# Kernel optimization log

Measured on AMD Instinct MI355X. Metric: run time of the kernel, lower is better.

## Reference

```python
import jax, jax.numpy as jnp
import numpy as np

B, N, F_IN, F_OUT = 64, 1024, 128, 64
NEG_BIG = -9e15


def setup_inputs() -> dict:
    key = jax.random.key(0)
    k1, k2, k3, k4 = jax.random.split(key, 4)
    atoms_vector = jax.random.normal(k1, (B, N, F_IN), dtype=jnp.float32)
    adjacency = jax.random.randint(k2, (B, N, N), 0, 2, dtype=jnp.int32)
    # xavier_uniform-ish init for params
    W = jax.random.uniform(k3, (F_IN, F_OUT), dtype=jnp.float32, minval=-1.0, maxval=1.0) * (1.414 * np.sqrt(6.0 / (F_IN + F_OUT)))
    a = jax.random.uniform(k4, (2 * F_OUT, 1), dtype=jnp.float32, minval=-1.0, maxval=1.0) * (1.414 * np.sqrt(6.0 / (2 * F_OUT + 1)))
    return {"atoms_vector": atoms_vector, "adjacency": adjacency, "W": W, "a": a}


def reference(atoms_vector, adjacency, W, a):
    f_out = W.shape[1]
    Wh = jnp.einsum('bni,io->bno', atoms_vector, W)  # (B, N, F_OUT)
    # The repeat_interleave/cat construction computes e[b,i,j] =
    # leaky_relu(a1 . Wh[b,i] + a2 . Wh[b,j]) — separable, so compute it directly.
    a1 = a[:f_out, 0]   # (F_OUT,)
    a2 = a[f_out:, 0]   # (F_OUT,)
    s1 = Wh @ a1        # (B, N)
    s2 = Wh @ a2        # (B, N)
    e = jax.nn.leaky_relu(s1[:, :, None] + s2[:, None, :], negative_slope=0.1)  # (B,N,N)
    attention = jnp.where(adjacency > 0, e, jnp.float32(NEG_BIG))
    attention = jax.nn.softmax(attention, axis=2)
    h_prime = jnp.einsum('bij,bjf->bif', attention, Wh)  # (B, N, F_OUT)
    return jax.nn.elu(h_prime)
```

## Files before the change

### kernel.cpp

```cpp
#include <hip/hip_runtime.h>
#include <hip/hip_bf16.h>

#define NN   1024
#define FIN  128
#define FOUT 64

typedef __attribute__((ext_vector_type(8))) short short8;
typedef __attribute__((ext_vector_type(4))) float f32x4;

__device__ inline unsigned short f2bf(float x) {
    union { __hip_bfloat16 h; unsigned short u; } c;
    c.h = __float2bfloat16(x);
    return c.u;
}
__device__ inline unsigned packbf(float a, float b) {
    return (unsigned)f2bf(a) | ((unsigned)f2bf(b) << 16);
}

__global__ __launch_bounds__(256) void k1_proj(
    const float* __restrict__ X, const float* __restrict__ W,
    const float* __restrict__ a,
    unsigned short* __restrict__ whbt,
    float* __restrict__ s1g, float* __restrict__ s2g)
{
    __shared__ float Ws[FIN][FOUT];
    __shared__ float Xs[64][FIN + 4];
    __shared__ unsigned short Ob[FOUT][64];

    const int t = threadIdx.x;
    const int blk = blockIdx.x;
    const int b = blk >> 4;
    const int r0 = (blk & 15) << 6;
    const float* Xg = X + ((size_t)(b * NN + r0)) * FIN;

    const float4* Wg4 = (const float4*)W;
    #pragma unroll
    for (int i = 0; i < 8; ++i) {
        int idx = t + i * 256;
        float4 v = Wg4[idx];
        int kk = idx >> 4, oo = (idx & 15) << 2;
        *(float4*)&Ws[kk][oo] = v;
    }
    #pragma unroll
    for (int i = 0; i < 8; ++i) {
        int idx = t + i * 256;
        float4 v = ((const float4*)Xg)[idx];
        int rr = idx >> 5, cc = (idx & 31) << 2;
        *(float4*)&Xs[rr][cc] = v;
    }
    __syncthreads();

    const int l = t & 63, w = t >> 6;
    const int c0 = (l & 15) << 2;
    const int rs = l >> 4;
    const int rbase = w * 16 + rs * 4;

    float acc[4][4] = {};
    for (int k = 0; k < FIN; ++k) {
        float4 wv = *(const float4*)&Ws[k][c0];
        #pragma unroll
        for (int q = 0; q < 4; ++q) {
            float x = Xs[rbase + q][k];
            acc[q][0] += x * wv.x; acc[q][1] += x * wv.y;
            acc[q][2] += x * wv.z; acc[q][3] += x * wv.w;
        }
    }

    float a1v[4], a2v[4];
    #pragma unroll
    for (int c = 0; c < 4; ++c) { a1v[c] = a[c0 + c]; a2v[c] = a[FOUT + c0 + c]; }
    #pragma unroll
    for (int q = 0; q < 4; ++q) {
        float p1 = acc[q][0]*a1v[0] + acc[q][1]*a1v[1] + acc[q][2]*a1v[2] + acc[q][3]*a1v[3];
        float p2 = acc[q][0]*a2v[0] + acc[q][1]*a2v[1] + acc[q][2]*a2v[2] + acc[q][3]*a2v[3];
        #pragma unroll
        for (int m = 1; m <= 8; m <<= 1) {
            p1 += __shfl_xor(p1, m, 64);
            p2 += __shfl_xor(p2, m, 64);
        }
        if ((l & 15) == 0) {
            int row = r0 + rbase + q;
            s1g[b * NN + row] = p1;
            s2g[b * NN + row] = p2;
        }
    }

    #pragma unroll
    for (int q = 0; q < 4; ++q)
        #pragma unroll
        for (int c = 0; c < 4; ++c)
            Ob[c0 + c][rbase + q] = f2bf(acc[q][c]);
    __syncthreads();

    {
        int o = t >> 2, rseg = (t & 3) << 4;
        unsigned short* dst = whbt + ((size_t)(b * FOUT + o)) * NN + r0 + rseg;
        const unsigned short* sp = &Ob[o][rseg];
        *(float4*)dst       = *(const float4*)sp;
        *(float4*)(dst + 8) = *(const float4*)(sp + 8);
    }
}

__global__ __launch_bounds__(256) void k1b_max(
    const float* __restrict__ s2g, float* __restrict__ s2max)
{
    int b = blockIdx.x, t = threadIdx.x;
    float m = -3.4e38f;
    #pragma unroll
    for (int i = 0; i < 4; ++i) m = fmaxf(m, s2g[b * NN + t + i * 256]);
    #pragma unroll
    for (int d = 1; d <= 32; d <<= 1) m = fmaxf(m, __shfl_xor(m, d, 64));
    __shared__ float red[4];
    if ((t & 63) == 0) red[t >> 6] = m;
    __syncthreads();
    if (t == 0) s2max[b] = fmaxf(fmaxf(red[0], red[1]), fmaxf(red[2], red[3]));
}

__global__ __launch_bounds__(256) void k2_attn(
    const int* __restrict__ adj,
    const unsigned short* __restrict__ whbt,
    const float* __restrict__ s1g, const float* __restrict__ s2g,
    const float* __restrict__ s2maxg,
    float* __restrict__ outg)
{
    const int t = threadIdx.x, l = t & 63, w = t >> 6;
    const int bid = blockIdx.x;
    const int b = bid >> 4;
    const int i0 = (bid & 15) << 6;
    const int r16 = l & 15;
    const int jo = (l >> 4) << 3;
    const int row = i0 + w * 16 + r16;

    const float s2m = s2maxg[b];
    const float s1v = s1g[b * NN + row];
    const float tt = s1v + s2m;
    const float Mr = fmaxf(tt, 0.1f * tt);

    const int* adjr = adj + (size_t)b * NN * NN + (size_t)row * NN;
    const float* s2r = s2g + b * NN;
    const unsigned short* wb = whbt + (size_t)b * FOUT * NN + (size_t)r16 * NN;

    f32x4 acc[4];
    #pragma unroll
    for (int s = 0; s < 4; ++s)
        #pragma unroll
        for (int r = 0; r < 4; ++r) acc[s][r] = 0.f;
    float den = 0.f;

    #pragma unroll 2
    for (int jt = 0; jt < NN; jt += 32) {
        const int j0 = jt + jo;
        int4 a0 = *(const int4*)(adjr + j0);
        int4 a1 = *(const int4*)(adjr + j0 + 4);
        float4 sa = *(const float4*)(s2r + j0);
        float4 sb = *(const float4*)(s2r + j0 + 4);
        short8 bf[4];
        #pragma unroll
        for (int s = 0; s < 4; ++s)
            bf[s] = *(const short8*)(wb + (size_t)s * (16 * NN) + j0);

        const float sv[8] = {sa.x, sa.y, sa.z, sa.w, sb.x, sb.y, sb.z, sb.w};
        const int   am[8] = {a0.x, a0.y, a0.z, a0.w, a1.x, a1.y, a1.z, a1.w};
        unsigned pk[4];
        #pragma unroll
        for (int e = 0; e < 4; ++e) {
            float xa = s1v + sv[2*e];
            float xb = s1v + sv[2*e+1];
            float ea = fmaxf(xa, 0.1f * xa) - Mr;
            float eb = fmaxf(xb, 0.1f * xb) - Mr;
            float pa = am[2*e]   > 0 ? __expf(ea) : 0.f;
            float pb = am[2*e+1] > 0 ? __expf(eb) : 0.f;
            den += pa + pb;
            pk[e] = packbf(pa, pb);
        }
        union { unsigned u[4]; short8 s8; } A;
        A.u[0] = pk[0]; A.u[1] = pk[1]; A.u[2] = pk[2]; A.u[3] = pk[3];
        #pragma unroll
        for (int s = 0; s < 4; ++s)
            acc[s] = __builtin_amdgcn_mfma_f32_16x16x32_bf16(A.s8, bf[s], acc[s], 0, 0, 0);
    }

    den += __shfl_xor(den, 16, 64);
    den += __shfl_xor(den, 32, 64);

    const int rb = (l >> 4) << 2;
    float inv[4];
    #pragma unroll
    for (int rr = 0; rr < 4; ++rr) {
        float dd = __shfl(den, rb + rr, 64);
        inv[rr] = dd > 0.f ? 1.f / dd : 0.f;
    }
    float* orow = outg + ((size_t)(b * NN + i0 + w * 16 + rb)) * FOUT;
    #pragma unroll
    for (int s = 0; s < 4; ++s)
        #pragma unroll
        for (int rr = 0; rr < 4; ++rr) {
            float v = acc[s][rr] * inv[rr];
            float res = v > 0.f ? v : (__expf(v) - 1.f);
            orow[(size_t)rr * FOUT + s * 16 + r16] = res;
        }
}

extern "C" void kernel_launch(void* const* d_in, const int* in_sizes, int n_in,
                              void* d_out, int out_size, void* d_ws, size_t ws_size,
                              hipStream_t stream) {
    const float* atoms = (const float*)d_in[0];
    const int*   adj   = (const int*)d_in[1];
    const float* W     = (const float*)d_in[2];
    const float* a     = (const float*)d_in[3];
    float* out = (float*)d_out;

    unsigned short* whbt = (unsigned short*)d_ws;
    float* s1g    = (float*)((char*)d_ws + (8u << 20));
    float* s2g    = (float*)((char*)d_ws + (8u << 20) + (256u << 10));
    float* s2maxg = (float*)((char*)d_ws + (8u << 20) + (512u << 10));

    k1_proj<<<1024, 256, 0, stream>>>(atoms, W, a, whbt, s1g, s2g);
    k1b_max<<<64, 256, 0, stream>>>(s2g, s2maxg);
    k2_attn<<<1024, 256, 0, stream>>>(adj, whbt, s1g, s2g, s2maxg, out);
}
```

Before: 127.8 us.

## Use MFMA bf16 for projection, fold attention vector into W, batch adjacency loads

Adds a tiny prep kernel that computes W·a1 and W·a2 and a transposed bf16 copy of W. The projection kernel then computes s1/s2 directly from X in fp32 and Wh with bf16 MFMA instructions, replacing the LDS-staged scalar FMA GEMM and the shared-memory transpose. The attention kernel now issues the adjacency loads for four 32-column chunks up front per 128-column step, to expose more memory-level parallelism. This trades fp32 accuracy for bf16 in Wh inputs and adds an extra kernel launch.

```diff
diff --git a/kernel.cpp b/kernel.cpp
--- a/kernel.cpp
+++ b/kernel.cpp
@@ -16,88 +16,93 @@
 __device__ inline unsigned packbf(float a, float b) {
     return (unsigned)f2bf(a) | ((unsigned)f2bf(b) << 16);
 }
+__device__ inline float dot4(float4 x, float4 y) {
+    return x.x*y.x + x.y*y.y + x.z*y.z + x.w*y.w;
+}
+
+__global__ __launch_bounds__(256) void k0_prep(
+    const float* __restrict__ W, const float* __restrict__ a,
+    float* __restrict__ wa1, float* __restrict__ wa2,
+    unsigned short* __restrict__ wtbf)
+{
+    const int t = threadIdx.x;
+    if (t < FIN) {
+        float s1 = 0.f, s2 = 0.f;
+        #pragma unroll
+        for (int c = 0; c < FOUT; c += 4) {
+            float4 wv  = *(const float4*)(W + t * FOUT + c);
+            float4 a1v = *(const float4*)(a + c);
+            float4 a2v = *(const float4*)(a + FOUT + c);
+            s1 += dot4(wv, a1v);
+            s2 += dot4(wv, a2v);
+        }
+        wa1[t] = s1; wa2[t] = s2;
+    }
+    const int col = t >> 2, ks = (t & 3) << 5;
+    #pragma unroll
+    for (int k = 0; k < 32; ++k)
+        wtbf[col * FIN + ks + k] = f2bf(W[(size_t)(ks + k) * FOUT + col]);
+}
 
 __global__ __launch_bounds__(256) void k1_proj(
-    const float* __restrict__ X, const float* __restrict__ W,
-    const float* __restrict__ a,
+    const float* __restrict__ X,
+    const float* __restrict__ wa1, const float* __restrict__ wa2,
+    const unsigned short* __restrict__ wtbf,
     unsigned short* __restrict__ whbt,
     float* __restrict__ s1g, float* __restrict__ s2g)
 {
-    __shared__ float Ws[FIN][FOUT];
-    __shared__ float Xs[64][FIN + 4];
-    __shared__ unsigned short Ob[FOUT][64];
-
-    const int t = threadIdx.x;
-    const int blk = blockIdx.x;
-    const int b = blk >> 4;
-    const int r0 = (blk & 15) << 6;
-    const float* Xg = X + ((size_t)(b * NN + r0)) * FIN;
-
-    const float4* Wg4 = (const float4*)W;
-    #pragma unroll
-    for (int i = 0; i < 8; ++i) {
-        int idx = t + i * 256;
-        float4 v = Wg4[idx];
-        int kk = idx >> 4, oo = (idx & 15) << 2;
-        *(float4*)&Ws[kk][oo] = v;
-    }
-    #pragma unroll
-    for (int i = 0; i < 8; ++i) {
-        int idx = t + i * 256;
-        float4 v = ((const float4*)Xg)[idx];
-        int rr = idx >> 5, cc = (idx & 31) << 2;
-        *(float4*)&Xs[rr][cc] = v;
-    }
-    __syncthreads();
-
-    const int l = t & 63, w = t >> 6;
-    const int c0 = (l & 15) << 2;
-    const int rs = l >> 4;
-    const int rbase = w * 16 + rs * 4;
-
-    float acc[4][4] = {};
-    for (int k = 0; k < FIN; ++k) {
-        float4 wv = *(const float4*)&Ws[k][c0];
-        #pragma unroll
-        for (int q = 0; q < 4; ++q) {
-            float x = Xs[rbase + q][k];
-            acc[q][0] += x * wv.x; acc[q][1] += x * wv.y;
-            acc[q][2] += x * wv.z; acc[q][3] += x * wv.w;
-        }
-    }
-
-    float a1v[4], a2v[4];
-    #pragma unroll
-    for (int c = 0; c < 4; ++c) { a1v[c] = a[c0 + c]; a2v[c] = a[FOUT + c0 + c]; }
-    #pragma unroll
-    for (int q = 0; q < 4; ++q) {
-        float p1 = acc[q][0]*a1v[0] + acc[q][1]*a1v[1] + acc[q][2]*a1v[2] + acc[q][3]*a1v[3];
-        float p2 = acc[q][0]*a2v[0] + acc[q][1]*a2v[1] + acc[q][2]*a2v[2] + acc[q][3]*a2v[3];
-        #pragma unroll
-        for (int m = 1; m <= 8; m <<= 1) {
-            p1 += __shfl_xor(p1, m, 64);
-            p2 += __shfl_xor(p2, m, 64);
-        }
-        if ((l & 15) == 0) {
-            int row = r0 + rbase + q;
-            s1g[b * NN + row] = p1;
-            s2g[b * NN + row] = p2;
-        }
-    }
-
-    #pragma unroll
-    for (int q = 0; q < 4; ++q)
-        #pragma unroll
-        for (int c = 0; c < 4; ++c)
-            Ob[c0 + c][rbase + q] = f2bf(acc[q][c]);
-    __syncthreads();
-
-    {
-        int o = t >> 2, rseg = (t & 3) << 4;
-        unsigned short* dst = whbt + ((size_t)(b * FOUT + o)) * NN + r0 + rseg;
-        const unsigned short* sp = &Ob[o][rseg];
-        *(float4*)dst       = *(const float4*)sp;
-        *(float4*)(dst + 8) = *(const float4*)(sp + 8);
+    const int t = threadIdx.x, l = t & 63, w = t >> 6;
+    const int bid = blockIdx.x;
+    const int b = bid >> 4;
+    const int r0 = (bid & 15) << 6;
+    const int r16 = l & 15;
+    const int jo = (l >> 4) << 3;
+    const int row = r0 + w * 16 + r16;
+    const float* xr = X + (size_t)(b * NN + row) * FIN;
+
+    f32x4 acc[4];
+    #pragma unroll
+    for (int s = 0; s < 4; ++s)
+        #pragma unroll
+        for (int r = 0; r < 4; ++r) acc[s][r] = 0.f;
+    float s1p = 0.f, s2p = 0.f;
+
+    #pragma unroll
+    for (int kc = 0; kc < 4; ++kc) {
+        const int k0i = kc * 32 + jo;
+        float4 xa = *(const float4*)(xr + k0i);
+        float4 xb = *(const float4*)(xr + k0i + 4);
+        float4 w1a = *(const float4*)(wa1 + k0i);
+        float4 w1b = *(const float4*)(wa1 + k0i + 4);
+        float4 w2a = *(const float4*)(wa2 + k0i);
+        float4 w2b = *(const float4*)(wa2 + k0i + 4);
+        s1p += dot4(xa, w1a) + dot4(xb, w1b);
+        s2p += dot4(xa, w2a) + dot4(xb, w2b);
+
+        union { unsigned u[4]; short8 s8; } A;
+        A.u[0] = packbf(xa.x, xa.y); A.u[1] = packbf(xa.z, xa.w);
+        A.u[2] = packbf(xb.x, xb.y); A.u[3] = packbf(xb.z, xb.w);
+        #pragma unroll
+        for (int s = 0; s < 4; ++s) {
+            short8 bfv = *(const short8*)(wtbf + (s * 16 + r16) * FIN + k0i);
+            acc[s] = __builtin_amdgcn_mfma_f32_16x16x32_bf16(A.s8, bfv, acc[s], 0, 0, 0);
+        }
+    }
+
+    s1p += __shfl_xor(s1p, 16, 64); s1p += __shfl_xor(s1p, 32, 64);
+    s2p += __shfl_xor(s2p, 16, 64); s2p += __shfl_xor(s2p, 32, 64);
+    if (jo == 0) {
+        s1g[b * NN + row] = s1p;
+        s2g[b * NN + row] = s2p;
+    }
+
+    const int rb = (l >> 4) << 2;
+    #pragma unroll
+    for (int s = 0; s < 4; ++s) {
+        unsigned d0 = packbf(acc[s][0], acc[s][1]);
+        unsigned d1 = packbf(acc[s][2], acc[s][3]);
+        *(uint2*)(whbt + (size_t)(b * FOUT + s * 16 + r16) * NN + r0 + w * 16 + rb)
+            = make_uint2(d0, d1);
     }
 }
 
@@ -147,37 +152,44 @@
         for (int r = 0; r < 4; ++r) acc[s][r] = 0.f;
     float den = 0.f;
 
-    #pragma unroll 2
-    for (int jt = 0; jt < NN; jt += 32) {
-        const int j0 = jt + jo;
-        int4 a0 = *(const int4*)(adjr + j0);
-        int4 a1 = *(const int4*)(adjr + j0 + 4);
-        float4 sa = *(const float4*)(s2r + j0);
-        float4 sb = *(const float4*)(s2r + j0 + 4);
-        short8 bf[4];
-        #pragma unroll
-        for (int s = 0; s < 4; ++s)
-            bf[s] = *(const short8*)(wb + (size_t)s * (16 * NN) + j0);
-
-        const float sv[8] = {sa.x, sa.y, sa.z, sa.w, sb.x, sb.y, sb.z, sb.w};
-        const int   am[8] = {a0.x, a0.y, a0.z, a0.w, a1.x, a1.y, a1.z, a1.w};
-        unsigned pk[4];
-        #pragma unroll
-        for (int e = 0; e < 4; ++e) {
-            float xa = s1v + sv[2*e];
-            float xb = s1v + sv[2*e+1];
-            float ea = fmaxf(xa, 0.1f * xa) - Mr;
-            float eb = fmaxf(xb, 0.1f * xb) - Mr;
-            float pa = am[2*e]   > 0 ? __expf(ea) : 0.f;
-            float pb = am[2*e+1] > 0 ? __expf(eb) : 0.f;
-            den += pa + pb;
-            pk[e] = packbf(pa, pb);
-        }
-        union { unsigned u[4]; short8 s8; } A;
-        A.u[0] = pk[0]; A.u[1] = pk[1]; A.u[2] = pk[2]; A.u[3] = pk[3];
-        #pragma unroll
-        for (int s = 0; s < 4; ++s)
-            acc[s] = __builtin_amdgcn_mfma_f32_16x16x32_bf16(A.s8, bf[s], acc[s], 0, 0, 0);
+    for (int jt = 0; jt < NN; jt += 128) {
+        int4 A0[4], A1[4];
+        #pragma unroll
+        for (int c = 0; c < 4; ++c) {
+            A0[c] = *(const int4*)(adjr + jt + c * 32 + jo);
+            A1[c] = *(const int4*)(adjr + jt + c * 32 + jo + 4);
+        }
+        #pragma unroll
+        for (int c = 0; c < 4; ++c) {
+            const int j0 = jt + c * 32 + jo;
+            float4 sa = *(const float4*)(s2r + j0);
+            float4 sb = *(const float4*)(s2r + j0 + 4);
+            short8 bfv[4];
+            #pragma unroll
+            for (int s = 0; s < 4; ++s)
+                bfv[s] = *(const short8*)(wb + (size_t)s * (16 * NN) + j0);
+
+            const float sv[8] = {sa.x, sa.y, sa.z, sa.w, sb.x, sb.y, sb.z, sb.w};
+            const int   am[8] = {A0[c].x, A0[c].y, A0[c].z, A0[c].w,
+                                 A1[c].x, A1[c].y, A1[c].z, A1[c].w};
+            unsigned pk[4];
+            #pragma unroll
+            for (int e = 0; e < 4; ++e) {
+                float xa = s1v + sv[2*e];
+                float xb = s1v + sv[2*e+1];
+                float ea = fmaxf(xa, 0.1f * xa) - Mr;
+                float eb = fmaxf(xb, 0.1f * xb) - Mr;
+                float pa = am[2*e]   > 0 ? __expf(ea) : 0.f;
+                float pb = am[2*e+1] > 0 ? __expf(eb) : 0.f;
+                den += pa + pb;
+                pk[e] = packbf(pa, pb);
+            }
+            union { unsigned u[4]; short8 s8; } A;
+            A.u[0] = pk[0]; A.u[1] = pk[1]; A.u[2] = pk[2]; A.u[3] = pk[3];
+            #pragma unroll
+            for (int s = 0; s < 4; ++s)
+                acc[s] = __builtin_amdgcn_mfma_f32_16x16x32_bf16(A.s8, bfv[s], acc[s], 0, 0, 0);
+        }
     }
 
     den += __shfl_xor(den, 16, 64);
@@ -210,12 +222,17 @@
     const float* a     = (const float*)d_in[3];
     float* out = (float*)d_out;
 
-    unsigned short* whbt = (unsigned short*)d_ws;
-    float* s1g    = (float*)((char*)d_ws + (8u << 20));
-    float* s2g    = (float*)((char*)d_ws + (8u << 20) + (256u << 10));
-    float* s2maxg = (float*)((char*)d_ws + (8u << 20) + (512u << 10));
-
-    k1_proj<<<1024, 256, 0, stream>>>(atoms, W, a, whbt, s1g, s2g);
+    char* ws = (char*)d_ws;
+    unsigned short* whbt   = (unsigned short*)ws;
+    float* s1g    = (float*)(ws + (8u << 20));
+    float* s2g    = (float*)(ws + (8u << 20) + (256u << 10));
+    float* s2maxg = (float*)(ws + (8u << 20) + (512u << 10));
+    float* wa1    = (float*)(ws + (8u << 20) + (513u << 10));
+    float* wa2    = (float*)(ws + (8u << 20) + (514u << 10));
+    unsigned short* wtbf = (unsigned short*)(ws + (8u << 20) + (515u << 10));
+
+    k0_prep<<<1, 256, 0, stream>>>(W, a, wa1, wa2, wtbf);
+    k1_proj<<<1024, 256, 0, stream>>>(atoms, wa1, wa2, wtbf, whbt, s1g, s2g);
     k1b_max<<<64, 256, 0, stream>>>(s2g, s2maxg);
     k2_attn<<<1024, 256, 0, stream>>>(adj, whbt, s1g, s2g, s2maxg, out);
 }
```

After: 131.4 us. +2.8%, slower.

## Pre-pack int32 adjacency into a bitmask before the attention kernel

Applied to the files above, without the earlier changes.

Adds a streaming kernel that compresses the int32 adjacency matrix into one bit per entry. The attention kernel then reads 128 bytes per row instead of 4 KB. The goal is to pull the large adjacency read out of the MFMA/exp loop, so the attention kernel works on compact data and the bulk read runs as a simple, fully coalesced stream. The cost is an extra launch and extra workspace writes and reads. The packing uses the low bit (`&1`) rather than `>0`, which is only equivalent for 0/1 adjacency values.

```diff
diff --git a/kernel.cpp b/kernel.cpp
--- a/kernel.cpp
+++ b/kernel.cpp
@@ -116,8 +116,27 @@
     if (t == 0) s2max[b] = fmaxf(fmaxf(red[0], red[1]), fmaxf(red[2], red[3]));
 }
 
-__global__ __launch_bounds__(256) void k2_attn(
-    const int* __restrict__ adj,
+__global__ __launch_bounds__(256) void k2a_pack(
+    const int* __restrict__ adj, unsigned char* __restrict__ mask)
+{
+    const size_t tid = (size_t)blockIdx.x * 256 + threadIdx.x;
+    const size_t nth = (size_t)gridDim.x * 256;
+    #pragma unroll 4
+    for (int it = 0; it < 16; ++it) {
+        size_t bp = tid + (size_t)it * nth;
+        const int* p = adj + bp * 8;
+        int4 a0 = *(const int4*)p;
+        int4 a1 = *(const int4*)(p + 4);
+        unsigned m = (unsigned)(a0.x & 1) | ((unsigned)(a0.y & 1) << 1)
+                   | ((unsigned)(a0.z & 1) << 2) | ((unsigned)(a0.w & 1) << 3)
+                   | ((unsigned)(a1.x & 1) << 4) | ((unsigned)(a1.y & 1) << 5)
+                   | ((unsigned)(a1.z & 1) << 6) | ((unsigned)(a1.w & 1) << 7);
+        mask[bp] = (unsigned char)m;
+    }
+}
+
+__global__ __launch_bounds__(256) void k2b_attn(
+    const unsigned char* __restrict__ maskg,
     const unsigned short* __restrict__ whbt,
     const float* __restrict__ s1g, const float* __restrict__ s2g,
     const float* __restrict__ s2maxg,
@@ -136,7 +155,7 @@
     const float tt = s1v + s2m;
     const float Mr = fmaxf(tt, 0.1f * tt);
 
-    const int* adjr = adj + (size_t)b * NN * NN + (size_t)row * NN;
+    const uint4* mrow = (const uint4*)(maskg + ((size_t)(b * NN) + row) * 128);
     const float* s2r = s2g + b * NN;
     const unsigned short* wb = whbt + (size_t)b * FOUT * NN + (size_t)r16 * NN;
 
@@ -147,37 +166,39 @@
         for (int r = 0; r < 4; ++r) acc[s][r] = 0.f;
     float den = 0.f;
 
-    #pragma unroll 2
-    for (int jt = 0; jt < NN; jt += 32) {
-        const int j0 = jt + jo;
-        int4 a0 = *(const int4*)(adjr + j0);
-        int4 a1 = *(const int4*)(adjr + j0 + 4);
-        float4 sa = *(const float4*)(s2r + j0);
-        float4 sb = *(const float4*)(s2r + j0 + 4);
-        short8 bf[4];
-        #pragma unroll
-        for (int s = 0; s < 4; ++s)
-            bf[s] = *(const short8*)(wb + (size_t)s * (16 * NN) + j0);
-
-        const float sv[8] = {sa.x, sa.y, sa.z, sa.w, sb.x, sb.y, sb.z, sb.w};
-        const int   am[8] = {a0.x, a0.y, a0.z, a0.w, a1.x, a1.y, a1.z, a1.w};
-        unsigned pk[4];
-        #pragma unroll
-        for (int e = 0; e < 4; ++e) {
-            float xa = s1v + sv[2*e];
-            float xb = s1v + sv[2*e+1];
-            float ea = fmaxf(xa, 0.1f * xa) - Mr;
-            float eb = fmaxf(xb, 0.1f * xb) - Mr;
-            float pa = am[2*e]   > 0 ? __expf(ea) : 0.f;
-            float pb = am[2*e+1] > 0 ? __expf(eb) : 0.f;
-            den += pa + pb;
-            pk[e] = packbf(pa, pb);
-        }
-        union { unsigned u[4]; short8 s8; } A;
-        A.u[0] = pk[0]; A.u[1] = pk[1]; A.u[2] = pk[2]; A.u[3] = pk[3];
-        #pragma unroll
-        for (int s = 0; s < 4; ++s)
-            acc[s] = __builtin_amdgcn_mfma_f32_16x16x32_bf16(A.s8, bf[s], acc[s], 0, 0, 0);
+    for (int jt = 0; jt < NN; jt += 128) {
+        uint4 mv = mrow[jt >> 7];
+        const unsigned mw[4] = {mv.x, mv.y, mv.z, mv.w};
+        #pragma unroll
+        for (int c = 0; c < 4; ++c) {
+            const int j0 = jt + c * 32 + jo;
+            const unsigned m8 = (mw[c] >> jo) & 0xffu;
+            float4 sa = *(const float4*)(s2r + j0);
+            float4 sb = *(const float4*)(s2r + j0 + 4);
+            short8 bfv[4];
+            #pragma unroll
+            for (int s = 0; s < 4; ++s)
+                bfv[s] = *(const short8*)(wb + (size_t)s * (16 * NN) + j0);
+
+            const float sv[8] = {sa.x, sa.y, sa.z, sa.w, sb.x, sb.y, sb.z, sb.w};
+            unsigned pk[4];
+            #pragma unroll
+            for (int e = 0; e < 4; ++e) {
+                float xa = s1v + sv[2*e];
+                float xb = s1v + sv[2*e+1];
+                float ea = fmaxf(xa, 0.1f * xa) - Mr;
+                float eb = fmaxf(xb, 0.1f * xb) - Mr;
+                float pa = (m8 >> (2*e))     & 1u ? __expf(ea) : 0.f;
+                float pb = (m8 >> (2*e + 1)) & 1u ? __expf(eb) : 0.f;
+                den += pa + pb;
+                pk[e] = packbf(pa, pb);
+            }
+            union { unsigned u[4]; short8 s8; } A;
+            A.u[0] = pk[0]; A.u[1] = pk[1]; A.u[2] = pk[2]; A.u[3] = pk[3];
+            #pragma unroll
+            for (int s = 0; s < 4; ++s)
+                acc[s] = __builtin_amdgcn_mfma_f32_16x16x32_bf16(A.s8, bfv[s], acc[s], 0, 0, 0);
+        }
     }
 
     den += __shfl_xor(den, 16, 64);
@@ -210,12 +231,15 @@
     const float* a     = (const float*)d_in[3];
     float* out = (float*)d_out;
 
-    unsigned short* whbt = (unsigned short*)d_ws;
-    float* s1g    = (float*)((char*)d_ws + (8u << 20));
-    float* s2g    = (float*)((char*)d_ws + (8u << 20) + (256u << 10));
-    float* s2maxg = (float*)((char*)d_ws + (8u << 20) + (512u << 10));
+    char* ws = (char*)d_ws;
+    unsigned short* whbt = (unsigned short*)ws;
+    float* s1g    = (float*)(ws + (8u << 20));
+    float* s2g    = (float*)(ws + (8u << 20) + (256u << 10));
+    float* s2maxg = (float*)(ws + (8u << 20) + (512u << 10));
+    unsigned char* mask = (unsigned char*)(ws + (9u << 20));
 
     k1_proj<<<1024, 256, 0, stream>>>(atoms, W, a, whbt, s1g, s2g);
     k1b_max<<<64, 256, 0, stream>>>(s2g, s2maxg);
-    k2_attn<<<1024, 256, 0, stream>>>(adj, whbt, s1g, s2g, s2maxg, out);
-}
+    k2a_pack<<<2048, 256, 0, stream>>>(adj, mask);
+    k2b_attn<<<1024, 256, 0, stream>>>(mask, whbt, s1g, s2g, s2maxg, out);
+}
```

After: 155.4 us. +21.6%, slower.
